# Kernel tuning notes

Hardware: AMD Instinct MI355X
Metric: run time of the kernel (lower is better)

The kernel has to match this reference:

```python
import jax, jax.numpy as jnp
import numpy as np

N_NODES = 50000
N_EDGES = 800000
D_IN = 64
D_OUT = 64


def setup_inputs() -> dict:
    key = jax.random.key(0)
    k = jax.random.split(key, 5)
    stdv = 1.0 / np.sqrt(D_OUT)
    X = jax.random.normal(k[0], (N_NODES, D_IN), jnp.float32)
    weights = jax.random.uniform(k[1], (D_IN, D_OUT), jnp.float32, -stdv, stdv)
    attention_w = jax.random.normal(k[2], (1, 1), jnp.float32)
    # edge list: row = destination (segment) ids, sorted (CSR-like); col = source ids
    row = jnp.sort(jax.random.randint(k[3], (N_EDGES,), 0, N_NODES, jnp.int32))
    col = jax.random.randint(k[4], (N_EDGES,), 0, N_NODES, jnp.int32)
    return {"X": X, "weights": weights, "attention_w": attention_w, "row": row, "col": col}


def reference(X, weights, attention_w, row, col):
    # dense linear
    Xp = X @ weights  # [N, D_OUT]
    # SDDMM: per-edge dot product between dst and src transformed features
    edge_feature = jnp.einsum('ed,ed->e', Xp[row], Xp[col])  # [E]
    # scale by scalar attention weight (n_heads = 1)
    edge_attn = edge_feature * attention_w[0, 0]  # [E]
    # SpMM aggregation: out[i] = sum_{e: row[e]=i} edge_attn[e] * Xp[col[e]]
    out = jax.ops.segment_sum(edge_attn[:, None] * Xp[col], row,
                              num_segments=X.shape[0])  # [N, D_OUT]
    return out
```

## Files before the change

kernel.cpp:

```cpp
#include <hip/hip_runtime.h>
#include <hip/hip_fp16.h>

#define D 64

typedef _Float16 h16;
typedef h16 h16x2 __attribute__((ext_vector_type(2)));

__device__ __forceinline__ h16x2 u2h(unsigned int u) {
    union { unsigned int i; h16x2 h; } t; t.i = u; return t.h;
}

__device__ __forceinline__ float dot8_f16(uint4 a, uint4 b, float c) {
#if __has_builtin(__builtin_amdgcn_fdot2)
    c = __builtin_amdgcn_fdot2(u2h(a.x), u2h(b.x), c, false);
    c = __builtin_amdgcn_fdot2(u2h(a.y), u2h(b.y), c, false);
    c = __builtin_amdgcn_fdot2(u2h(a.z), u2h(b.z), c, false);
    c = __builtin_amdgcn_fdot2(u2h(a.w), u2h(b.w), c, false);
    return c;
#else
    float2 t;
    t = __half22float2(*(const __half2*)&a.x); float2 s = __half22float2(*(const __half2*)&b.x);
    c = fmaf(t.x, s.x, c); c = fmaf(t.y, s.y, c);
    t = __half22float2(*(const __half2*)&a.y); s = __half22float2(*(const __half2*)&b.y);
    c = fmaf(t.x, s.x, c); c = fmaf(t.y, s.y, c);
    t = __half22float2(*(const __half2*)&a.z); s = __half22float2(*(const __half2*)&b.z);
    c = fmaf(t.x, s.x, c); c = fmaf(t.y, s.y, c);
    t = __half22float2(*(const __half2*)&a.w); s = __half22float2(*(const __half2*)&b.w);
    c = fmaf(t.x, s.x, c); c = fmaf(t.y, s.y, c);
    return c;
#endif
}

__device__ __forceinline__ void h8_to_f32(uint4 u, float f[8]) {
    float2 t;
    t = __half22float2(*(const __half2*)&u.x); f[0] = t.x; f[1] = t.y;
    t = __half22float2(*(const __half2*)&u.y); f[2] = t.x; f[3] = t.y;
    t = __half22float2(*(const __half2*)&u.z); f[4] = t.x; f[5] = t.y;
    t = __half22float2(*(const __half2*)&u.w); f[6] = t.x; f[7] = t.y;
}

__global__ __launch_bounds__(256) void prep_kernel(const float* __restrict__ X,
                                                   const float* __restrict__ W,
                                                   const int* __restrict__ row,
                                                   __half* __restrict__ Xp,
                                                   int* __restrict__ rowptr,
                                                   int nNodes, int nEdges,
                                                   int gemmBlocks) {
    if ((int)blockIdx.x >= gemmBlocks) {
        int e = (blockIdx.x - gemmBlocks) * 256 + threadIdx.x;
        if (e >= nEdges) return;
        int r = row[e];
        int rprev = (e == 0) ? -1 : row[e - 1];
        for (int q = rprev + 1; q <= r; ++q) rowptr[q] = e;
        if (e == nEdges - 1) {
            for (int q = r + 1; q <= nNodes; ++q) rowptr[q] = nEdges;
        }
        return;
    }
    int lane = threadIdx.x & 63;
    int wave = (blockIdx.x * 256 + threadIdx.x) >> 6;
    int nWaves = gemmBlocks * 4;

    float w[D];
#pragma unroll
    for (int k = 0; k < D; ++k) w[k] = W[k * D + lane];

    for (int r = wave; r < nNodes; r += nWaves) {
        int rr = __builtin_amdgcn_readfirstlane(r);
        const float4* xr = (const float4*)(X + (size_t)rr * D);
        float acc = 0.f;
#pragma unroll
        for (int k4 = 0; k4 < D / 4; ++k4) {
            float4 xv = xr[k4];
            acc = fmaf(xv.x, w[4 * k4 + 0], acc);
            acc = fmaf(xv.y, w[4 * k4 + 1], acc);
            acc = fmaf(xv.z, w[4 * k4 + 2], acc);
            acc = fmaf(xv.w, w[4 * k4 + 3], acc);
        }
        Xp[(size_t)rr * D + lane] = __float2half(acc);
    }
}

__global__ __launch_bounds__(256) void fused_kernel(const __half* __restrict__ Xp,
                                                    const int* __restrict__ rowptr,
                                                    const int* __restrict__ col,
                                                    const float* __restrict__ attn_w,
                                                    float* __restrict__ out,
                                                    int nNodes) {
    int lane = threadIdx.x & 63;
    int waveId = (blockIdx.x * 256 + threadIdx.x) >> 6;
    int g = lane >> 3;
    int j = lane & 7;

    int node = waveId * 8 + g;
    bool active = node < nNodes;
    int nd = active ? node : 0;

    int eStart = rowptr[nd];
    int eEnd   = active ? rowptr[nd + 1] : eStart;

    const uint4* XpV = (const uint4*)Xp;
    uint4 xr = XpV[(size_t)nd * 8 + j];

    float acc[8] = {0.f, 0.f, 0.f, 0.f, 0.f, 0.f, 0.f, 0.f};

    bool v[4]; uint4 raw[4];
#pragma unroll
    for (int u = 0; u < 4; ++u) {
        int ee = eStart + u;
        v[u] = ee < eEnd;
        int cc = col[v[u] ? ee : 0];
        raw[u] = XpV[(size_t)cc * 8 + j];
    }

    for (int e = eStart; e < eEnd; e += 4) {
        bool v2[4]; uint4 raw2[4];
#pragma unroll
        for (int u = 0; u < 4; ++u) {
            int ee = e + 4 + u;
            v2[u] = ee < eEnd;
            int cc = col[v2[u] ? ee : 0];
            raw2[u] = XpV[(size_t)cc * 8 + j];
        }
        float p[4];
#pragma unroll
        for (int u = 0; u < 4; ++u) p[u] = dot8_f16(xr, raw[u], 0.f);
#pragma unroll
        for (int off = 1; off < 8; off <<= 1)
#pragma unroll
            for (int u = 0; u < 4; ++u) p[u] += __shfl_xor(p[u], off, 64);
#pragma unroll
        for (int u = 0; u < 4; ++u) {
            float s = v[u] ? p[u] : 0.f;
            float xf[8]; h8_to_f32(raw[u], xf);
#pragma unroll
            for (int q = 0; q < 8; ++q) acc[q] = fmaf(s, xf[q], acc[q]);
        }
#pragma unroll
        for (int u = 0; u < 4; ++u) { v[u] = v2[u]; raw[u] = raw2[u]; }
    }

    if (active) {
        float attn = attn_w[0];
        float4* o = (float4*)(out + (size_t)node * D + 8 * j);
        o[0] = make_float4(attn * acc[0], attn * acc[1], attn * acc[2], attn * acc[3]);
        o[1] = make_float4(attn * acc[4], attn * acc[5], attn * acc[6], attn * acc[7]);
    }
}

extern "C" void kernel_launch(void* const* d_in, const int* in_sizes, int n_in,
                              void* d_out, int out_size, void* d_ws, size_t ws_size,
                              hipStream_t stream) {
    const float* X    = (const float*)d_in[0];
    const float* W    = (const float*)d_in[1];
    const float* attn = (const float*)d_in[2];
    const int*   row  = (const int*)d_in[3];
    const int*   col  = (const int*)d_in[4];
    float* out = (float*)d_out;

    int nNodes = in_sizes[0] / D;
    int nEdges = in_sizes[3];

    __half* Xp  = (__half*)d_ws;
    int* rowptr = (int*)((char*)d_ws + (size_t)nNodes * D * sizeof(__half));

    int gemmBlocks = 1024;
    int rpBlocks   = (nEdges + 255) / 256;
    prep_kernel<<<gemmBlocks + rpBlocks, 256, 0, stream>>>(X, W, row, Xp, rowptr,
                                                           nNodes, nEdges, gemmBlocks);

    int waves = (nNodes + 7) / 8;
    fused_kernel<<<(waves + 3) / 4, 256, 0, stream>>>(Xp, rowptr, col, attn, out, nNodes);
}
```

Baseline: 104.8 us.

## Use persistent atomic work queue and fp16 packed accumulation in fused SDDMM-SpMM

The fused kernel becomes persistent with 1024 blocks. Each wave pulls groups of eight nodes from a global atomic counter, which the prep kernel resets, so uneven per-node degree is balanced dynamically. The per-edge aggregation now accumulates in packed half2 with hfma2 instead of converting to fp32 and using scalar FMAs. This cuts conversion and FMA instruction count, but fp16 accumulation loses precision and can overflow. The atomic fetch also adds a small cost per node group.

```diff
diff --git a/kernel.cpp b/kernel.cpp
--- a/kernel.cpp
+++ b/kernel.cpp
@@ -18,8 +18,8 @@
     c = __builtin_amdgcn_fdot2(u2h(a.w), u2h(b.w), c, false);
     return c;
 #else
-    float2 t;
-    t = __half22float2(*(const __half2*)&a.x); float2 s = __half22float2(*(const __half2*)&b.x);
+    float2 t, s;
+    t = __half22float2(*(const __half2*)&a.x); s = __half22float2(*(const __half2*)&b.x);
     c = fmaf(t.x, s.x, c); c = fmaf(t.y, s.y, c);
     t = __half22float2(*(const __half2*)&a.y); s = __half22float2(*(const __half2*)&b.y);
     c = fmaf(t.x, s.x, c); c = fmaf(t.y, s.y, c);
@@ -31,21 +31,16 @@
 #endif
 }
 
-__device__ __forceinline__ void h8_to_f32(uint4 u, float f[8]) {
-    float2 t;
-    t = __half22float2(*(const __half2*)&u.x); f[0] = t.x; f[1] = t.y;
-    t = __half22float2(*(const __half2*)&u.y); f[2] = t.x; f[3] = t.y;
-    t = __half22float2(*(const __half2*)&u.z); f[4] = t.x; f[5] = t.y;
-    t = __half22float2(*(const __half2*)&u.w); f[6] = t.x; f[7] = t.y;
-}
-
 __global__ __launch_bounds__(256) void prep_kernel(const float* __restrict__ X,
                                                    const float* __restrict__ W,
                                                    const int* __restrict__ row,
                                                    __half* __restrict__ Xp,
                                                    int* __restrict__ rowptr,
+                                                   int* __restrict__ workCtr,
                                                    int nNodes, int nEdges,
                                                    int gemmBlocks) {
+    if (blockIdx.x == 0 && threadIdx.x == 0) *workCtr = 0;
+
     if ((int)blockIdx.x >= gemmBlocks) {
         int e = (blockIdx.x - gemmBlocks) * 256 + threadIdx.x;
         if (e >= nEdges) return;
@@ -85,66 +80,80 @@
                                                     const int* __restrict__ rowptr,
                                                     const int* __restrict__ col,
                                                     const float* __restrict__ attn_w,
+                                                    int* __restrict__ workCtr,
                                                     float* __restrict__ out,
                                                     int nNodes) {
     int lane = threadIdx.x & 63;
-    int waveId = (blockIdx.x * 256 + threadIdx.x) >> 6;
     int g = lane >> 3;
     int j = lane & 7;
+    int nOct = (nNodes + 7) >> 3;
+    float attn = attn_w[0];
+    const uint4* XpV = (const uint4*)Xp;
 
-    int node = waveId * 8 + g;
-    bool active = node < nNodes;
-    int nd = active ? node : 0;
+    for (;;) {
+        int oct;
+        if (lane == 0) oct = atomicAdd(workCtr, 1);
+        oct = __shfl(oct, 0, 64);
+        if (oct >= nOct) break;
 
-    int eStart = rowptr[nd];
-    int eEnd   = active ? rowptr[nd + 1] : eStart;
+        int node = oct * 8 + g;
+        bool active = node < nNodes;
+        int nd = active ? node : 0;
 
-    const uint4* XpV = (const uint4*)Xp;
-    uint4 xr = XpV[(size_t)nd * 8 + j];
+        int eStart = rowptr[nd];
+        int eEnd   = active ? rowptr[nd + 1] : eStart;
 
-    float acc[8] = {0.f, 0.f, 0.f, 0.f, 0.f, 0.f, 0.f, 0.f};
+        uint4 xr = XpV[(size_t)nd * 8 + j];
 
-    bool v[4]; uint4 raw[4];
+        __half2 acc[4];
 #pragma unroll
-    for (int u = 0; u < 4; ++u) {
-        int ee = eStart + u;
-        v[u] = ee < eEnd;
-        int cc = col[v[u] ? ee : 0];
-        raw[u] = XpV[(size_t)cc * 8 + j];
-    }
+        for (int q = 0; q < 4; ++q) acc[q] = __float2half2_rn(0.f);
 
-    for (int e = eStart; e < eEnd; e += 4) {
-        bool v2[4]; uint4 raw2[4];
+        bool v[4]; uint4 raw[4];
 #pragma unroll
         for (int u = 0; u < 4; ++u) {
-            int ee = e + 4 + u;
-            v2[u] = ee < eEnd;
-            int cc = col[v2[u] ? ee : 0];
-            raw2[u] = XpV[(size_t)cc * 8 + j];
+            int ee = eStart + u;
+            v[u] = ee < eEnd;
+            int cc = col[v[u] ? ee : 0];
+            raw[u] = XpV[(size_t)cc * 8 + j];
         }
-        float p[4];
+
+        for (int e = eStart; e < eEnd; e += 4) {
+            bool v2[4]; uint4 raw2[4];
 #pragma unroll
-        for (int u = 0; u < 4; ++u) p[u] = dot8_f16(xr, raw[u], 0.f);
+            for (int u = 0; u < 4; ++u) {
+                int ee = e + 4 + u;
+                v2[u] = ee < eEnd;
+                int cc = col[v2[u] ? ee : 0];
+                raw2[u] = XpV[(size_t)cc * 8 + j];
+            }
+            float p[4];
 #pragma unroll
-        for (int off = 1; off < 8; off <<= 1)
+            for (int u = 0; u < 4; ++u) p[u] = dot8_f16(xr, raw[u], 0.f);
 #pragma unroll
-            for (int u = 0; u < 4; ++u) p[u] += __shfl_xor(p[u], off, 64);
+            for (int off = 1; off < 8; off <<= 1)
 #pragma unroll
-        for (int u = 0; u < 4; ++u) {
-            float s = v[u] ? p[u] : 0.f;
-            float xf[8]; h8_to_f32(raw[u], xf);
+                for (int u = 0; u < 4; ++u) p[u] += __shfl_xor(p[u], off, 64);
 #pragma unroll
-            for (int q = 0; q < 8; ++q) acc[q] = fmaf(s, xf[q], acc[q]);
+            for (int u = 0; u < 4; ++u) {
+                __half2 sh = __float2half2_rn(v[u] ? p[u] : 0.f);
+                const __half2* xh = (const __half2*)&raw[u];
+#pragma unroll
+                for (int q = 0; q < 4; ++q) acc[q] = __hfma2(sh, xh[q], acc[q]);
+            }
+#pragma unroll
+            for (int u = 0; u < 4; ++u) { v[u] = v2[u]; raw[u] = raw2[u]; }
         }
-#pragma unroll
-        for (int u = 0; u < 4; ++u) { v[u] = v2[u]; raw[u] = raw2[u]; }
-    }
 
-    if (active) {
-        float attn = attn_w[0];
-        float4* o = (float4*)(out + (size_t)node * D + 8 * j);
-        o[0] = make_float4(attn * acc[0], attn * acc[1], attn * acc[2], attn * acc[3]);
-        o[1] = make_float4(attn * acc[4], attn * acc[5], attn * acc[6], attn * acc[7]);
+        if (active) {
+            float2 f0 = __half22float2(acc[0]);
+            float2 f1 = __half22float2(acc[1]);
+            float2 f2 = __half22float2(acc[2]);
+            float2 f3 = __half22float2(acc[3]);
+            float4* o = (float4*)(out + (size_t)node * D + 8 * j);
+            o[0] = make_float4(attn * f0.x, attn * f0.y, attn * f1.x, attn * f1.y);
+            o[1] = make_float4(attn * f2.x, attn * f2.y, attn * f3.x, attn * f3.y);
+        }
     }
 }
 
@@ -163,12 +172,13 @@
 
     __half* Xp  = (__half*)d_ws;
     int* rowptr = (int*)((char*)d_ws + (size_t)nNodes * D * sizeof(__half));
+    int* workCtr = rowptr + (nNodes + 1);
 
     int gemmBlocks = 1024;
     int rpBlocks   = (nEdges + 255) / 256;
     prep_kernel<<<gemmBlocks + rpBlocks, 256, 0, stream>>>(X, W, row, Xp, rowptr,
-                                                           nNodes, nEdges, gemmBlocks);
+                                                           workCtr, nNodes, nEdges,
+                                                           gemmBlocks);
 
-    int waves = (nNodes + 7) / 8;
-    fused_kernel<<<(waves + 3) / 4, 256, 0, stream>>>(Xp, rowptr, col, attn, out, nNodes);
+    fused_kernel<<<1024, 256, 0, stream>>>(Xp, rowptr, col, attn, workCtr, out, nNodes);
 }
```

After: 211.9 us. +102.2%, slower.
